# Optimization experiments

Hardware: AMD Instinct MI355X
Metric: run time of the kernel (lower is better)

Reference implementation:

```python
import jax, jax.numpy as jnp
import numpy as np

B, N, D, H, K = 16, 256, 64, 64, 2  # batch, nodes, d_in, d_hidden, top_k


def setup_inputs() -> dict:
    key = jax.random.key(0)
    k0, k1, k2 = jax.random.split(key, 3)
    O = jax.random.normal(k0, (B, N, D), dtype=jnp.float32)
    # PairwiseFeaturizer.proj: Linear(4*D, H) -> ReLU -> Linear(H, 1)
    W1 = jax.random.normal(k1, (4 * D, H), dtype=jnp.float32) / np.sqrt(4 * D).astype(np.float32)
    b1 = jnp.zeros((H,), dtype=jnp.float32)
    W2 = jax.random.normal(k2, (H, 1), dtype=jnp.float32) / np.sqrt(H).astype(np.float32)
    b2 = jnp.zeros((1,), dtype=jnp.float32)
    return {"O": O, "W1": W1, "b1": b1, "W2": W2, "b2": b2}


def reference(O, W1, b1, W2, b2):
    Bn, Nn, d = O.shape
    ii, jj = jnp.triu_indices(Nn, k=1)  # all undirected pairs i<j, M = N(N-1)/2
    Oi = O[:, ii, :]  # (B, M, d) gather
    Oj = O[:, jj, :]  # (B, M, d) gather
    feats = jnp.concatenate([Oi, Oj, jnp.abs(Oi - Oj), Oi * Oj], axis=-1)  # (B, M, 4d)
    h = jax.nn.relu(jnp.einsum('bmf,fh->bmh', feats, W1) + b1)
    Q = (jnp.einsum('bmh,ho->bmo', h, W2) + b2)[..., 0]  # (B, M)
    # greedy top-k selection mask (eps -> 0 limit of select_pairs)
    idx = jax.lax.top_k(Q, K)[1]  # (B, K)
    mask = jnp.zeros(Q.shape, dtype=bool).at[jnp.arange(Q.shape[0])[:, None], idx].set(True)
    return Q, mask
```

## Files before the change

### kernel.cpp

```cpp
#include <hip/hip_runtime.h>
#include <math.h>

#define Bn 16
#define Nn 256
#define Mm (Nn*(Nn-1)/2)
#define CHUNK 4080

typedef __attribute__((ext_vector_type(8))) short bf16x8;
typedef __attribute__((ext_vector_type(4))) short short4v;
typedef __attribute__((ext_vector_type(4))) float f32x4;

typedef union { bf16x8 v; short s[8]; __bf16 h[8]; } F8;
typedef union { short4v v; __bf16 h[4]; } F4;

#define MFMA(acc, a, b) \
  acc = __builtin_amdgcn_mfma_f32_16x16x32_bf16((a), (b), (acc), 0, 0, 0)

__device__ __forceinline__ void top2_update(float v, int m,
    float& v1, int& i1, float& v2, int& i2)
{
  bool c1 = (v > v1) || (v == v1 && m < i1);
  bool c2 = (v > v2) || (v == v2 && m < i2);
  float nv2 = c1 ? v1 : (c2 ? v : v2);
  int   ni2 = c1 ? i1 : (c2 ? m : i2);
  v1 = c1 ? v : v1;  i1 = c1 ? m : i1;
  v2 = nv2;          i2 = ni2;
}

__global__ __launch_bounds__(256) void prep_w1t(
    const float* __restrict__ W1, unsigned short* __restrict__ wtg)
{
  const int h = blockIdx.x;
  const int k = threadIdx.x;
  __bf16 b = (__bf16)W1[k * 64 + h];
  wtg[h * 256 + k] = *(unsigned short*)&b;
}

__global__ __launch_bounds__(256, 3) void pair_kernel(
    const float* __restrict__ O,
    const float* __restrict__ b1,
    const float* __restrict__ W2,
    const float* __restrict__ b2,
    const unsigned short* __restrict__ wtg,
    float* __restrict__ Q,
    float* __restrict__ cand)
{
  __shared__ __align__(16) unsigned short s_oi[16][72];
  __shared__ __align__(16) unsigned short s_oj[32][72];
  __shared__ float s_A[16][68];
  __shared__ float s_C[32][68];
  __shared__ float s_q[16][36];
  __shared__ float s_w2[64];
  __shared__ float s_red[4][4];

  const int t  = threadIdx.x;
  const int l  = t & 63, wv = t >> 6;
  const int lo = l & 15, g = l >> 4;

  const int blk   = blockIdx.x;
  const int batch = blk / 72;
  int tl          = blk % 72;
  int a = 0;
  while (tl >= 8 - (a >> 1)) { tl -= 8 - (a >> 1); ++a; }
  const int c   = (a >> 1) + tl;
  const int ti0 = a * 16, tj0 = c * 32;

  const float* Ob = O + (size_t)batch * Nn * 64;

  {
    const float4* Oi4 = (const float4*)(Ob + ti0 * 64);
    {
      int r = t >> 4, c4 = (t & 15) * 4;
      float4 x = Oi4[t];
      F4 p; p.h[0] = (__bf16)x.x; p.h[1] = (__bf16)x.y;
            p.h[2] = (__bf16)x.z; p.h[3] = (__bf16)x.w;
      *(short4v*)&s_oi[r][c4] = p.v;
    }
    const float4* Oj4 = (const float4*)(Ob + tj0 * 64);
    #pragma unroll
    for (int p2 = 0; p2 < 2; ++p2) {
      int v = t + p2 * 256;
      int r = v >> 4, c4 = (v & 15) * 4;
      float4 x = Oj4[v];
      F4 p; p.h[0] = (__bf16)x.x; p.h[1] = (__bf16)x.y;
            p.h[2] = (__bf16)x.z; p.h[3] = (__bf16)x.w;
      *(short4v*)&s_oj[r][c4] = p.v;
    }
    if (t < 64) s_w2[t] = W2[t];
  }
  __syncthreads();

  if (wv < 2) {
    #pragma unroll
    for (int nn = 0; nn < 2; ++nn) {
      const int nf = wv * 2 + nn;
      f32x4 ac = {0.f, 0.f, 0.f, 0.f};
      #pragma unroll
      for (int ks = 0; ks < 2; ++ks) {
        F8 aop; aop.v = *(const bf16x8*)&s_oi[lo][ks * 32 + g * 8];
        F8 bop; bop.v = *(const bf16x8*)&wtg[(nf * 16 + lo) * 256 + ks * 32 + g * 8];
        MFMA(ac, aop.v, bop.v);
      }
      const float bb = b1[nf * 16 + lo];
      #pragma unroll
      for (int r = 0; r < 4; ++r)
        s_A[g * 4 + r][nf * 16 + lo] = ac[r] + bb;
    }
  } else {
    const int mf = wv - 2;
    #pragma unroll
    for (int nf = 0; nf < 4; ++nf) {
      f32x4 ac = {0.f, 0.f, 0.f, 0.f};
      #pragma unroll
      for (int ks = 0; ks < 2; ++ks) {
        F8 aop; aop.v = *(const bf16x8*)&s_oj[mf * 16 + lo][ks * 32 + g * 8];
        F8 bop; bop.v = *(const bf16x8*)&wtg[(nf * 16 + lo) * 256 + 64 + ks * 32 + g * 8];
        MFMA(ac, aop.v, bop.v);
      }
      #pragma unroll
      for (int r = 0; r < 4; ++r)
        s_C[mf * 16 + g * 4 + r][nf * 16 + lo] = ac[r];
    }
  }

  F8 bfr[4][4];
  #pragma unroll
  for (int ks = 0; ks < 4; ++ks)
    #pragma unroll
    for (int nf = 0; nf < 4; ++nf)
      bfr[ks][nf].v = *(const bf16x8*)&wtg[(nf * 16 + lo) * 256 + 128 + ks * 32 + g * 8];

  __syncthreads();

  for (int ii = 0; ii < 4; ++ii) {
    const int iL = wv * 4 + ii;

    f32x4 as4[4];
    #pragma unroll
    for (int nf = 0; nf < 4; ++nf)
      as4[nf] = *(const f32x4*)&s_A[iL][nf * 16 + g * 4];

    float oiv[16];
    {
      F8 u0, u1;
      u0.v = *(const bf16x8*)&s_oi[iL][g * 8];
      u1.v = *(const bf16x8*)&s_oi[iL][32 + g * 8];
      #pragma unroll
      for (int e = 0; e < 8; ++e) {
        oiv[e]     = (float)u0.h[e];
        oiv[8 + e] = (float)u1.h[e];
      }
    }

    #pragma unroll
    for (int jh = 0; jh < 2; ++jh) {
      F8 fb0, fb1, fb2, fb3;
      {
        F8 v0, v1;
        v0.v = *(const bf16x8*)&s_oj[jh * 16 + lo][g * 8];
        v1.v = *(const bf16x8*)&s_oj[jh * 16 + lo][32 + g * 8];
        #pragma unroll
        for (int e = 0; e < 8; ++e) {
          float p0 = (float)v0.h[e], p1 = (float)v1.h[e];
          float d0 = oiv[e] - p0,    d1 = oiv[8 + e] - p1;
          fb0.h[e] = (__bf16)fabsf(d0);
          fb1.h[e] = (__bf16)fabsf(d1);
          fb2.h[e] = (__bf16)(oiv[e] * p0);
          fb3.h[e] = (__bf16)(oiv[8 + e] * p1);
        }
      }

      f32x4 acc0, acc1, acc2, acc3;
      {
        f32x4 c0 = *(const f32x4*)&s_C[jh * 16 + lo][0 * 16 + g * 4];
        f32x4 c1 = *(const f32x4*)&s_C[jh * 16 + lo][1 * 16 + g * 4];
        f32x4 c2 = *(const f32x4*)&s_C[jh * 16 + lo][2 * 16 + g * 4];
        f32x4 c3 = *(const f32x4*)&s_C[jh * 16 + lo][3 * 16 + g * 4];
        acc0 = as4[0] + c0; acc1 = as4[1] + c1;
        acc2 = as4[2] + c2; acc3 = as4[3] + c3;
      }

      MFMA(acc0, bfr[0][0].v, fb0.v); MFMA(acc1, bfr[0][1].v, fb0.v);
      MFMA(acc2, bfr[0][2].v, fb0.v); MFMA(acc3, bfr[0][3].v, fb0.v);
      MFMA(acc0, bfr[1][0].v, fb1.v); MFMA(acc1, bfr[1][1].v, fb1.v);
      MFMA(acc2, bfr[1][2].v, fb1.v); MFMA(acc3, bfr[1][3].v, fb1.v);
      MFMA(acc0, bfr[2][0].v, fb2.v); MFMA(acc1, bfr[2][1].v, fb2.v);
      MFMA(acc2, bfr[2][2].v, fb2.v); MFMA(acc3, bfr[2][3].v, fb2.v);
      MFMA(acc0, bfr[3][0].v, fb3.v); MFMA(acc1, bfr[3][1].v, fb3.v);
      MFMA(acc2, bfr[3][2].v, fb3.v); MFMA(acc3, bfr[3][3].v, fb3.v);

      float part = 0.f;
      {
        f32x4 w0 = *(const f32x4*)&s_w2[0 * 16 + g * 4];
        f32x4 w1 = *(const f32x4*)&s_w2[1 * 16 + g * 4];
        f32x4 w2q = *(const f32x4*)&s_w2[2 * 16 + g * 4];
        f32x4 w3 = *(const f32x4*)&s_w2[3 * 16 + g * 4];
        #pragma unroll
        for (int r = 0; r < 4; ++r) {
          part = fmaf(fmaxf(acc0[r], 0.f), w0[r], part);
          part = fmaf(fmaxf(acc1[r], 0.f), w1[r], part);
          part = fmaf(fmaxf(acc2[r], 0.f), w2q[r], part);
          part = fmaf(fmaxf(acc3[r], 0.f), w3[r], part);
        }
      }
      part += __shfl_xor(part, 16);
      part += __shfl_xor(part, 32);
      if (g == 0) s_q[iL][jh * 16 + lo] = part;
    }
  }
  __syncthreads();

  {
    const float b2v = b2[0];
    const int e0 = t * 2;
    const int row = e0 >> 5, col0 = e0 & 31;
    const int i = ti0 + row;
    float v1 = -INFINITY, v2 = -INFINITY;
    int   i1 = 0x7fffffff, i2 = 0x7fffffff;
    const int mbase = i * (Nn - 1) - (i * (i - 1)) / 2 - i - 1;
    #pragma unroll
    for (int e = 0; e < 2; ++e) {
      const int col = col0 + e;
      const int j = tj0 + col;
      const float qv = s_q[row][col] + b2v;
      if (j > i) {
        const int m = mbase + j;
        Q[(size_t)batch * Mm + m] = qv;
        top2_update(qv, m, v1, i1, v2, i2);
      }
    }
    #pragma unroll
    for (int s = 1; s < 64; s <<= 1) {
      float u1 = __shfl_xor(v1, s); int j1 = __shfl_xor(i1, s);
      float u2 = __shfl_xor(v2, s); int j2 = __shfl_xor(i2, s);
      top2_update(u1, j1, v1, i1, v2, i2);
      top2_update(u2, j2, v1, i1, v2, i2);
    }
    if (l == 0) {
      s_red[wv][0] = v1; s_red[wv][1] = __int_as_float(i1);
      s_red[wv][2] = v2; s_red[wv][3] = __int_as_float(i2);
    }
    __syncthreads();
    if (t == 0) {
      float a1 = s_red[0][0]; int x1 = __float_as_int(s_red[0][1]);
      float a2 = s_red[0][2]; int x2 = __float_as_int(s_red[0][3]);
      #pragma unroll
      for (int e = 1; e < 4; ++e) {
        top2_update(s_red[e][0], __float_as_int(s_red[e][1]), a1, x1, a2, x2);
        top2_update(s_red[e][2], __float_as_int(s_red[e][3]), a1, x1, a2, x2);
      }
      float* cp = cand + (size_t)blk * 4;
      cp[0] = a1; cp[1] = __int_as_float(x1);
      cp[2] = a2; cp[3] = __int_as_float(x2);
    }
  }
}

__global__ __launch_bounds__(256) void rank_kernel(
    const float* __restrict__ O, const float* __restrict__ W1,
    const float* __restrict__ b1, const float* __restrict__ W2,
    const float* __restrict__ cand, int* __restrict__ ws2)
{
  const int b = blockIdx.x;
  const int t = threadIdx.x;
  __shared__ float s_cv[144];
  __shared__ int   s_ci[144];
  __shared__ int   s_m[8];
  __shared__ int   s_ij[8][2];
  __shared__ float s_or[8][2][64];
  __shared__ float s_part[8][32];
  __shared__ float s_qe[8];

  if (t < 144) {
    const float* cp = cand + (size_t)(b * 72 + (t >> 1)) * 4;
    s_cv[t] = cp[(t & 1) * 2];
    s_ci[t] = __float_as_int(cp[(t & 1) * 2 + 1]);
  }
  __syncthreads();
  if (t < 144) {
    float v = s_cv[t]; int m = s_ci[t];
    int rank = 0;
    for (int e = 0; e < 144; ++e) {
      float u = s_cv[e]; int n = s_ci[e];
      rank += (u > v || (u == v && n < m)) ? 1 : 0;
    }
    if (rank < 8) s_m[rank] = m;
  }
  __syncthreads();
  if (t < 16) {
    int m = s_m[t >> 1];
    int i = 0, rem = m;
    while (rem >= Nn - 1 - i) { rem -= Nn - 1 - i; ++i; }
    int j = i + 1 + rem;
    s_ij[t >> 1][t & 1] = (t & 1) ? j : i;
  }
  __syncthreads();
  {
    int c = t >> 5, rr = (t >> 4) & 1, c4 = (t & 15) * 4;
    int row = s_ij[c][rr];
    *(float4*)&s_or[c][rr][c4] = *(const float4*)&O[((size_t)b * Nn + row) * 64 + c4];
  }
  __syncthreads();
  {
    int c = t >> 5, hh = t & 31, h2 = hh * 2;
    float z0 = b1[h2], z1 = b1[h2 + 1];
    for (int d = 0; d < 64; ++d) {
      float oi = s_or[c][0][d], oj = s_or[c][1][d];
      float f3 = fabsf(oi - oj), f4 = oi * oj;
      float2 wa = *(const float2*)&W1[(d      ) * 64 + h2];
      float2 wb = *(const float2*)&W1[(64 + d ) * 64 + h2];
      float2 wc = *(const float2*)&W1[(128 + d) * 64 + h2];
      float2 wd = *(const float2*)&W1[(192 + d) * 64 + h2];
      z0 += oi * wa.x + oj * wb.x + f3 * wc.x + f4 * wd.x;
      z1 += oi * wa.y + oj * wb.y + f3 * wc.y + f4 * wd.y;
    }
    s_part[c][hh] = fmaxf(z0, 0.f) * W2[h2] + fmaxf(z1, 0.f) * W2[h2 + 1];
  }
  __syncthreads();
  if (t < 8) {
    float s = 0.f;
    for (int e = 0; e < 32; ++e) s += s_part[t][e];
    s_qe[t] = s;
  }
  __syncthreads();
  if (t == 0) {
    float v1 = -INFINITY, v2 = -INFINITY;
    int   i1 = 0x7fffffff, i2 = 0x7fffffff;
    for (int e = 0; e < 8; ++e)
      top2_update(s_qe[e], s_m[e], v1, i1, v2, i2);
    ws2[b * 2] = i1; ws2[b * 2 + 1] = i2;
  }
}

__global__ __launch_bounds__(256) void mask_kernel(
    const int* __restrict__ ws2, float* __restrict__ mask)
{
  const int b = blockIdx.x >> 3, cch = blockIdx.x & 7, t = threadIdx.x;
  const int k0 = ws2[b * 2], k1 = ws2[b * 2 + 1];
  float* mb = mask + (size_t)b * Mm;
  const int m0 = cch * CHUNK;
  for (int m = m0 + t; m < m0 + CHUNK; m += 256)
    mb[m] = (m == k0 || m == k1) ? 1.0f : 0.0f;
}

extern "C" void kernel_launch(void* const* d_in, const int* in_sizes, int n_in,
                              void* d_out, int out_size, void* d_ws, size_t ws_size,
                              hipStream_t stream) {
  const float* O  = (const float*)d_in[0];
  const float* W1 = (const float*)d_in[1];
  const float* b1 = (const float*)d_in[2];
  const float* W2 = (const float*)d_in[3];
  const float* b2 = (const float*)d_in[4];

  float* Q    = (float*)d_out;
  float* mask = Q + (size_t)Bn * Mm;

  unsigned short* wtg = (unsigned short*)d_ws;
  float* cand = (float*)((char*)d_ws + 32768);
  int*   ws2  = (int*)((char*)d_ws + 32768 + 18432);

  prep_w1t<<<dim3(64), dim3(256), 0, stream>>>(W1, wtg);
  pair_kernel<<<dim3(Bn * 72), dim3(256), 0, stream>>>(O, b1, W2, b2, wtg, Q, cand);
  rank_kernel<<<dim3(Bn), dim3(256), 0, stream>>>(O, W1, b1, W2, cand, ws2);
  mask_kernel<<<dim3(Bn * 8), dim3(256), 0, stream>>>(ws2, mask);
}
```

Baseline: 59.45 us.

## Fuse rank and mask kernels, hoist Oj/C loads out of pair loop

```diff
diff --git a/kernel.cpp b/kernel.cpp
--- a/kernel.cpp
+++ b/kernel.cpp
@@ -36,7 +36,7 @@
   wtg[h * 256 + k] = *(unsigned short*)&b;
 }
 
-__global__ __launch_bounds__(256, 3) void pair_kernel(
+__global__ __launch_bounds__(256, 4) void pair_kernel(
     const float* __restrict__ O,
     const float* __restrict__ b1,
     const float* __restrict__ W2,
@@ -132,6 +132,26 @@
 
   __syncthreads();
 
+  float ojv[2][16];
+  #pragma unroll
+  for (int jh = 0; jh < 2; ++jh) {
+    F8 u0, u1;
+    u0.v = *(const bf16x8*)&s_oj[jh * 16 + lo][g * 8];
+    u1.v = *(const bf16x8*)&s_oj[jh * 16 + lo][32 + g * 8];
+    #pragma unroll
+    for (int e = 0; e < 8; ++e) {
+      ojv[jh][e]     = (float)u0.h[e];
+      ojv[jh][8 + e] = (float)u1.h[e];
+    }
+  }
+  f32x4 cin[2][4];
+  #pragma unroll
+  for (int jh = 0; jh < 2; ++jh)
+    #pragma unroll
+    for (int nf = 0; nf < 4; ++nf)
+      cin[jh][nf] = *(const f32x4*)&s_C[jh * 16 + lo][nf * 16 + g * 4];
+
+  #pragma unroll
   for (int ii = 0; ii < 4; ++ii) {
     const int iL = wv * 4 + ii;
 
@@ -155,30 +175,20 @@
     #pragma unroll
     for (int jh = 0; jh < 2; ++jh) {
       F8 fb0, fb1, fb2, fb3;
-      {
-        F8 v0, v1;
-        v0.v = *(const bf16x8*)&s_oj[jh * 16 + lo][g * 8];
-        v1.v = *(const bf16x8*)&s_oj[jh * 16 + lo][32 + g * 8];
-        #pragma unroll
-        for (int e = 0; e < 8; ++e) {
-          float p0 = (float)v0.h[e], p1 = (float)v1.h[e];
-          float d0 = oiv[e] - p0,    d1 = oiv[8 + e] - p1;
-          fb0.h[e] = (__bf16)fabsf(d0);
-          fb1.h[e] = (__bf16)fabsf(d1);
-          fb2.h[e] = (__bf16)(oiv[e] * p0);
-          fb3.h[e] = (__bf16)(oiv[8 + e] * p1);
-        }
-      }
-
-      f32x4 acc0, acc1, acc2, acc3;
-      {
-        f32x4 c0 = *(const f32x4*)&s_C[jh * 16 + lo][0 * 16 + g * 4];
-        f32x4 c1 = *(const f32x4*)&s_C[jh * 16 + lo][1 * 16 + g * 4];
-        f32x4 c2 = *(const f32x4*)&s_C[jh * 16 + lo][2 * 16 + g * 4];
-        f32x4 c3 = *(const f32x4*)&s_C[jh * 16 + lo][3 * 16 + g * 4];
-        acc0 = as4[0] + c0; acc1 = as4[1] + c1;
-        acc2 = as4[2] + c2; acc3 = as4[3] + c3;
-      }
+      #pragma unroll
+      for (int e = 0; e < 8; ++e) {
+        float p0 = ojv[jh][e], p1 = ojv[jh][8 + e];
+        float d0 = oiv[e] - p0,    d1 = oiv[8 + e] - p1;
+        fb0.h[e] = (__bf16)fabsf(d0);
+        fb1.h[e] = (__bf16)fabsf(d1);
+        fb2.h[e] = (__bf16)(oiv[e] * p0);
+        fb3.h[e] = (__bf16)(oiv[8 + e] * p1);
+      }
+
+      f32x4 acc0 = as4[0] + cin[jh][0];
+      f32x4 acc1 = as4[1] + cin[jh][1];
+      f32x4 acc2 = as4[2] + cin[jh][2];
+      f32x4 acc3 = as4[3] + cin[jh][3];
 
       MFMA(acc0, bfr[0][0].v, fb0.v); MFMA(acc1, bfr[0][1].v, fb0.v);
       MFMA(acc2, bfr[0][2].v, fb0.v); MFMA(acc3, bfr[0][3].v, fb0.v);
@@ -256,20 +266,21 @@
   }
 }
 
-__global__ __launch_bounds__(256) void rank_kernel(
+__global__ __launch_bounds__(256) void rankmask_kernel(
     const float* __restrict__ O, const float* __restrict__ W1,
     const float* __restrict__ b1, const float* __restrict__ W2,
-    const float* __restrict__ cand, int* __restrict__ ws2)
+    const float* __restrict__ cand, float* __restrict__ mask)
 {
-  const int b = blockIdx.x;
-  const int t = threadIdx.x;
+  const int b   = blockIdx.x >> 3;
+  const int cch = blockIdx.x & 7;
+  const int t   = threadIdx.x;
   __shared__ float s_cv[144];
   __shared__ int   s_ci[144];
   __shared__ int   s_m[8];
   __shared__ int   s_ij[8][2];
   __shared__ float s_or[8][2][64];
   __shared__ float s_part[8][32];
-  __shared__ float s_qe[8];
+  __shared__ int   s_k0, s_k1;
 
   if (t < 144) {
     const float* cp = cand + (size_t)(b * 72 + (t >> 1)) * 4;
@@ -296,16 +307,17 @@
   }
   __syncthreads();
   {
-    int c = t >> 5, rr = (t >> 4) & 1, c4 = (t & 15) * 4;
-    int row = s_ij[c][rr];
-    *(float4*)&s_or[c][rr][c4] = *(const float4*)&O[((size_t)b * Nn + row) * 64 + c4];
+    int cc = t >> 5, rr = (t >> 4) & 1, c4 = (t & 15) * 4;
+    int row = s_ij[cc][rr];
+    *(float4*)&s_or[cc][rr][c4] = *(const float4*)&O[((size_t)b * Nn + row) * 64 + c4];
   }
   __syncthreads();
   {
-    int c = t >> 5, hh = t & 31, h2 = hh * 2;
+    int cc = t >> 5, hh = t & 31, h2 = hh * 2;
     float z0 = b1[h2], z1 = b1[h2 + 1];
+    #pragma unroll 8
     for (int d = 0; d < 64; ++d) {
-      float oi = s_or[c][0][d], oj = s_or[c][1][d];
+      float oi = s_or[cc][0][d], oj = s_or[cc][1][d];
       float f3 = fabsf(oi - oj), f4 = oi * oj;
       float2 wa = *(const float2*)&W1[(d      ) * 64 + h2];
       float2 wb = *(const float2*)&W1[(64 + d ) * 64 + h2];
@@ -314,29 +326,22 @@
       z0 += oi * wa.x + oj * wb.x + f3 * wc.x + f4 * wd.x;
       z1 += oi * wa.y + oj * wb.y + f3 * wc.y + f4 * wd.y;
     }
-    s_part[c][hh] = fmaxf(z0, 0.f) * W2[h2] + fmaxf(z1, 0.f) * W2[h2 + 1];
-  }
-  __syncthreads();
-  if (t < 8) {
-    float s = 0.f;
-    for (int e = 0; e < 32; ++e) s += s_part[t][e];
-    s_qe[t] = s;
+    s_part[cc][hh] = fmaxf(z0, 0.f) * W2[h2] + fmaxf(z1, 0.f) * W2[h2 + 1];
   }
   __syncthreads();
   if (t == 0) {
     float v1 = -INFINITY, v2 = -INFINITY;
     int   i1 = 0x7fffffff, i2 = 0x7fffffff;
-    for (int e = 0; e < 8; ++e)
-      top2_update(s_qe[e], s_m[e], v1, i1, v2, i2);
-    ws2[b * 2] = i1; ws2[b * 2 + 1] = i2;
-  }
-}
-
-__global__ __launch_bounds__(256) void mask_kernel(
-    const int* __restrict__ ws2, float* __restrict__ mask)
-{
-  const int b = blockIdx.x >> 3, cch = blockIdx.x & 7, t = threadIdx.x;
-  const int k0 = ws2[b * 2], k1 = ws2[b * 2 + 1];
+    for (int e = 0; e < 8; ++e) {
+      float s = 0.f;
+      for (int u = 0; u < 32; ++u) s += s_part[e][u];
+      top2_update(s, s_m[e], v1, i1, v2, i2);
+    }
+    s_k0 = i1; s_k1 = i2;
+  }
+  __syncthreads();
+
+  const int k0 = s_k0, k1 = s_k1;
   float* mb = mask + (size_t)b * Mm;
   const int m0 = cch * CHUNK;
   for (int m = m0 + t; m < m0 + CHUNK; m += 256)
@@ -357,10 +362,8 @@
 
   unsigned short* wtg = (unsigned short*)d_ws;
   float* cand = (float*)((char*)d_ws + 32768);
-  int*   ws2  = (int*)((char*)d_ws + 32768 + 18432);
 
   prep_w1t<<<dim3(64), dim3(256), 0, stream>>>(W1, wtg);
   pair_kernel<<<dim3(Bn * 72), dim3(256), 0, stream>>>(O, b1, W2, b2, wtg, Q, cand);
-  rank_kernel<<<dim3(Bn), dim3(256), 0, stream>>>(O, W1, b1, W2, cand, ws2);
-  mask_kernel<<<dim3(Bn * 8), dim3(256), 0, stream>>>(ws2, mask);
-}
+  rankmask_kernel<<<dim3(Bn * 8), dim3(256), 0, stream>>>(O, W1, b1, W2, cand, mask);
+}
```

Result: slower. 178.4 us (+200.1%).
